# Kernel optimization log

Hardware: AMD Instinct MI355X
Metric: run time of the kernel (lower is better)

## Reference

```python
import jax, jax.numpy as jnp
import numpy as np
import math

B, D, N, H, NHEADS, NCLS = 4096, 256, 256, 1, 4, 10


def conv(x, w, b, stride, pad):
    y = jax.lax.conv_general_dilated(x, w, (stride, stride), [(pad, pad), (pad, pad)],
                                     dimension_numbers=('NCHW', 'OIHW', 'NCHW'))
    return y + b[None, :, None, None]


def cdist(z, c):
    # z: [B, D], c: [N, D] -> Euclidean distance [B, N]
    d2 = jnp.sum(z * z, -1)[:, None] + jnp.sum(c * c, -1)[None, :] - 2.0 * (z @ c.T)
    return jnp.sqrt(jnp.maximum(d2, 0.0))


def setup_inputs() -> dict:
    key = jax.random.key(0)
    ks = jax.random.split(key, 32)
    s = 0.02
    inp = {
        'x': jax.random.normal(ks[0], (B, 3, 32, 32), jnp.float32),
        'y': jax.random.randint(ks[1], (B,), 0, NCLS),
        'conv1_w': jax.random.normal(ks[2], (32, 3, 5, 5), jnp.float32) * s,
        'conv1_b': jnp.zeros((32,), jnp.float32),
        'conv2_w': jax.random.normal(ks[3], (64, 32, 3, 3), jnp.float32) * s,
        'conv2_b': jnp.zeros((64,), jnp.float32),
        'conv3_w': jax.random.normal(ks[4], (128, 64, 3, 3), jnp.float32) * s,
        'conv3_b': jnp.zeros((128,), jnp.float32),
        'conv4_w': jax.random.normal(ks[5], (256, 128, 3, 3), jnp.float32) * s,
        'conv4_b': jnp.zeros((256,), jnp.float32),
        'enc_w': jax.random.normal(ks[6], (256 * 8 * 8, D), jnp.float32) * s,
        'enc_b': jnp.zeros((D,), jnp.float32),
        'class_emb': jax.random.normal(ks[7], (NCLS, D), jnp.float32),
        'node_emb': jax.random.normal(ks[8], (N_NODES := 1, D), jnp.float32),
        'query_w': jax.random.normal(ks[9], (D, D), jnp.float32) * s,
        'query_b': jnp.zeros((D,), jnp.float32),
        'attn_w': jax.random.normal(ks[10], (D, D * NHEADS), jnp.float32) * s,
        'attn_b': jnp.zeros((D * NHEADS,), jnp.float32),
        'clf_w': jax.random.normal(ks[11], (D * NHEADS, NCLS), jnp.float32) * s,
        'clf_b': jnp.zeros((NCLS,), jnp.float32),
        'node_fc_w': jax.random.normal(ks[12], (D, D), jnp.float32) * s,
        'node_fc_b': jnp.zeros((D,), jnp.float32),
        'protos': jax.random.normal(ks[13], (N, D), jnp.float32),
        'grid_pos': jax.random.normal(ks[14], (N, D), jnp.float32),
        'temp_raw': jnp.array([math.log(0.95 / 0.05)], jnp.float32),
        'gate_logits': jnp.zeros((N,), jnp.float32),
    }
    return inp


def reference(x, y, conv1_w, conv1_b, conv2_w, conv2_b, conv3_w, conv3_b,
              conv4_w, conv4_b, enc_w, enc_b, class_emb, node_emb,
              query_w, query_b, attn_w, attn_b, clf_w, clf_b,
              node_fc_w, node_fc_b, protos, grid_pos, temp_raw, gate_logits):
    # shared encoder: conv stack -> flatten -> linear, 32x32 -> 8x8
    h1 = jax.nn.relu(conv(x, conv1_w, conv1_b, 2, 1))    # [B,32,15,15]
    h2 = jax.nn.relu(conv(h1, conv2_w, conv2_b, 2, 1))   # [B,64,8,8]
    h3 = jax.nn.relu(conv(h2, conv3_w, conv3_b, 1, 1))   # [B,128,8,8]
    h4 = jax.nn.relu(conv(h3, conv4_w, conv4_b, 1, 1))   # [B,256,8,8]
    z0 = h4.reshape(x.shape[0], -1) @ enc_w + enc_b      # [B,D]

    # Node: encoder_fc + SoftSOM (cdist + cdist -> softmax -> gate -> renorm -> blend)
    z = z0 @ node_fc_w + node_fc_b
    temp = jax.nn.sigmoid(temp_raw[0]) * (1.0 - 0.001) + 0.001
    d_total = cdist(z, protos) + cdist(z, grid_pos)      # [B,N]
    w = jax.nn.softmax(-d_total / temp, axis=-1) * jax.nn.sigmoid(gate_logits)[None, :]
    w = w / (w.sum(-1, keepdims=True) + 1e-8)
    blended = w @ protos                                 # [B,D]

    # node attention over n_nodes=1
    topo_stack = blended[:, None, :]                     # [B,1,D]
    query = class_emb[y] @ query_w + query_b             # [B,D]
    proj = (node_emb @ attn_w + attn_b).reshape(node_emb.shape[0], NHEADS, D)  # [n,h,D]
    attn_logits = jnp.einsum('bd,nhd->bhn', query, proj)
    attn_w_ = jax.nn.softmax(attn_logits, axis=-1)
    fused = jnp.einsum('bhn,bnd->bhd', attn_w_, topo_stack).reshape(x.shape[0], NHEADS * D)
    logits = fused @ clf_w + clf_b                       # [B,10]
    return logits
```

## Files before the change

kernel.cpp:

```cpp
#include <hip/hip_runtime.h>
#include <math.h>

#define TPB 256

typedef __attribute__((ext_vector_type(8))) short bf16x8;
typedef __attribute__((ext_vector_type(4))) float f32x4;
typedef __attribute__((ext_vector_type(2))) float f32x2;

#define OFF_PN2   0
#define OFF_GN2   256
#define OFF_GATE  512
#define OFF_TEMP  768
#define OFF_WEFF  1024
#define OFF_W1T   3584
#define OFF_W2T_BYTES 737280ul
#define OFF_W3T_BYTES 786432ul
#define OFF_W4T_BYTES 983040ul
#define OFF_EWT_BYTES 2097152ul
#define OFF_NFWT_BYTES 10485760ul
#define OFF_PJD_BYTES  10616832ul
#define OFF_GJD_BYTES  10747904ul
#define OFF_PTB_BYTES  10878976ul
#define OFF_A_BYTES   12582912ul
#define OFF_B_BYTES   (OFF_A_BYTES + 67108864ul)
#define OFF_Z0_BYTES  (OFF_B_BYTES + 33554432ul)

__device__ __forceinline__ float bf2f(ushort u) {
  return __uint_as_float(((unsigned)u) << 16);
}
__device__ __forceinline__ ushort f2bf(float f) {
  unsigned x = __float_as_uint(f);
  return (ushort)((x + 0x7fffu + ((x >> 16) & 1u)) >> 16);
}
__device__ __forceinline__ unsigned pack2(float a, float b) {
  return (unsigned)f2bf(a) | ((unsigned)f2bf(b) << 16);
}

__device__ __forceinline__ void gload_lds16(const ushort* g, ushort* l) {
  __builtin_amdgcn_global_load_lds(
      (const __attribute__((address_space(1))) unsigned int*)g,
      (__attribute__((address_space(3))) unsigned int*)l, 16, 0, 0);
}

__device__ __forceinline__ float block_sum(float v, float* red) {
  #pragma unroll
  for (int off = 32; off > 0; off >>= 1) v += __shfl_down(v, off, 64);
  int wid = threadIdx.x >> 6;
  __syncthreads();
  if ((threadIdx.x & 63) == 0) red[wid] = v;
  __syncthreads();
  return red[0] + red[1] + red[2] + red[3];
}

__global__ void __launch_bounds__(256) k_init(
    const float* __restrict__ ew,    ushort* __restrict__ ewt,
    const float* __restrict__ w1,    const float* __restrict__ w2,
    const float* __restrict__ w3,    const float* __restrict__ w4,
    float* __restrict__ w1t, ushort* __restrict__ w2t,
    ushort* __restrict__ w3t, ushort* __restrict__ w4t,
    const float* __restrict__ protos, const float* __restrict__ gridp,
    const float* __restrict__ gate_logits, const float* __restrict__ temp_raw,
    const float* __restrict__ clf_w, float* __restrict__ ws,
    float* __restrict__ z0,
    const float* __restrict__ nfw, ushort* __restrict__ nfwt,
    ushort* __restrict__ pjd, ushort* __restrict__ gjd,
    ushort* __restrict__ ptb) {
  __shared__ float tile[64][65];
  __shared__ float red[4];
  const int bx = blockIdx.x, t = threadIdx.x;

  if (bx < 1024) {
    int kb = bx & 255, nb = bx >> 8;
    #pragma unroll
    for (int i = 0; i < 16; ++i) {
      int idx = t + i*256, k = idx >> 6, n = idx & 63;
      tile[k][n] = ew[(size_t)(kb*64 + k)*256 + nb*64 + n];
    }
    __syncthreads();
    #pragma unroll
    for (int i = 0; i < 16; ++i) {
      int idx = t + i*256, n = idx >> 6, k = idx & 63;
      ewt[(size_t)(nb*64 + n)*16384 + kb*64 + k] = f2bf(tile[k][n]);
    }
    return;
  }
  if (bx < 2176) {
    int idx = (bx - 1024)*256 + t;
    if (idx < 2400) {
      int tap = idx >> 5, oc = idx & 31;
      w1t[idx] = w1[oc*75 + tap];
    }
    if (idx < 18432) {
      int tap = idx >> 11, r = idx & 2047, oc = r >> 5, ic = r & 31;
      w2t[idx] = f2bf(w2[oc*288 + ic*9 + tap]);
    }
    if (idx < 73728) {
      int tap = idx >> 13, r = idx & 8191, oc = r >> 6, ic = r & 63;
      w3t[idx] = f2bf(w3[oc*576 + ic*9 + tap]);
    }
    if (idx < 294912) {
      int tap = idx >> 15, r = idx & 32767, oc = r >> 7, ic = r & 127;
      w4t[idx] = f2bf(w4[oc*1152 + ic*9 + tap]);
    }
    return;
  }
  if (bx < 2432) {
    int b = bx - 2176;
    #pragma unroll
    for (int u = 0; u < 16; ++u) z0[(size_t)u*65536 + b*256 + t] = 0.f;
    float pv = protos[b*256 + t];
    float gv = gridp [b*256 + t];
    float sp = block_sum(pv*pv, red);
    float sg = block_sum(gv*gv, red);
    if (t == 0) {
      ws[OFF_PN2 + b] = sp;
      ws[OFF_GN2 + b] = sg;
      ws[OFF_GATE + b] = 1.f/(1.f + expf(-gate_logits[b]));
    }
    if (b == 0) {
      for (int i = t; i < 2560; i += TPB) {
        int d = i/10, c = i%10;
        ws[OFF_WEFF + i] = clf_w[d*10+c] + clf_w[(256+d)*10+c]
                         + clf_w[(512+d)*10+c] + clf_w[(768+d)*10+c];
      }
      if (t == 0) {
        float s = 1.f/(1.f + expf(-temp_raw[0]));
        ws[OFF_TEMP] = s*(1.f - 0.001f) + 0.001f;
      }
    }
    return;
  }
  {
    int idx = (bx - 2432)*256 + t;
    int a = idx >> 8, b = idx & 255;
    nfwt[idx] = f2bf(nfw[b*256 + a]);
    pjd [idx] = f2bf(protos[idx]);
    gjd [idx] = f2bf(gridp[idx]);
    ptb [idx] = f2bf(protos[b*256 + a]);
  }
}

__global__ void __launch_bounds__(256) k_conv12(const float* __restrict__ x,
    const float* __restrict__ w1t, const float* __restrict__ b1,
    const ushort* __restrict__ w2t, const float* __restrict__ b2,
    ushort* __restrict__ h2c) {
  __shared__ ushort xs[17*17*40];
  int b = blockIdx.x, t = threadIdx.x;
  for (int i = t; i < 5780; i += TPB) ((unsigned*)xs)[i] = 0u;
  const float* xb = x + (size_t)b*3072;

  if (t < 225) {
    int oy = t/15, ox = t%15;
    f32x2 acc[16];
    #pragma unroll
    for (int o = 0; o < 16; ++o) acc[o] = *(const f32x2*)&b1[2*o];
    for (int ic = 0; ic < 3; ++ic) {
      const int icb = ic*1024;
      #pragma unroll
      for (int ky = 0; ky < 5; ++ky) {
        int iy = 2*oy - 1 + ky;
        bool rok = (unsigned)iy < 32u;
        int rbase = icb + (rok ? iy*32 : 0);
        #pragma unroll
        for (int kx = 0; kx < 5; ++kx) {
          int ix = 2*ox - 1 + kx;
          bool ok = rok && ((unsigned)ix < 32u);
          float xv = xb[rbase + (ok ? ix : 0)];
          xv = ok ? xv : 0.f;
          f32x2 xv2 = {xv, xv};
          const float* wrow = &w1t[(ic*25 + ky*5 + kx)*32];
          #pragma unroll
          for (int g = 0; g < 8; ++g) {
            f32x2 wlo = {wrow[4*g+0], wrow[4*g+1]};
            f32x2 whi = {wrow[4*g+2], wrow[4*g+3]};
            acc[2*g]   += xv2*wlo;
            acc[2*g+1] += xv2*whi;
          }
        }
      }
    }
    unsigned pk[16];
    #pragma unroll
    for (int g = 0; g < 16; ++g)
      pk[g] = pack2(fmaxf(acc[g].x, 0.f), fmaxf(acc[g].y, 0.f));
    ushort* cell = &xs[((oy+1)*17 + (ox+1))*40];
    #pragma unroll
    for (int q = 0; q < 4; ++q) *(uint4*)(cell + q*8) = ((uint4*)pk)[q];
  }
  __syncthreads();

  const int lane = t & 63, w = t >> 6;
  const int quad = lane >> 4, row16 = lane & 15;
  f32x4 acc2[4];
  #pragma unroll
  for (int mt = 0; mt < 4; ++mt) acc2[mt] = (f32x4)0.f;
  #pragma unroll
  for (int ky = 0; ky < 3; ++ky)
    #pragma unroll
    for (int kx = 0; kx < 3; ++kx) {
      int tap = ky*3 + kx;
      bf16x8 bf = *(const bf16x8*)&w2t[tap*2048 + (w*16 + row16)*32 + quad*8];
      #pragma unroll
      for (int mt = 0; mt < 4; ++mt) {
        int px = mt*16 + row16;
        int iy = 2*(px >> 3) + ky, ix = 2*(px & 7) + kx;
        bf16x8 af = *(const bf16x8*)&xs[(iy*17 + ix)*40 + quad*8];
        acc2[mt] = __builtin_amdgcn_mfma_f32_16x16x32_bf16(bf, af, acc2[mt], 0, 0, 0);
      }
    }
  float4 bb = *(const float4*)&b2[w*16 + quad*4];
  #pragma unroll
  for (int mt = 0; mt < 4; ++mt) {
    int px = mt*16 + row16;
    uint2 dd;
    dd.x = pack2(fmaxf(acc2[mt][0] + bb.x, 0.f), fmaxf(acc2[mt][1] + bb.y, 0.f));
    dd.y = pack2(fmaxf(acc2[mt][2] + bb.z, 0.f), fmaxf(acc2[mt][3] + bb.w, 0.f));
    *(uint2*)&h2c[(size_t)b*4096 + px*64 + w*16 + quad*4] = dd;
  }
}

__global__ void __launch_bounds__(256, 2) k_conv34(const ushort* __restrict__ h2c,
    const float* __restrict__ b3, const float* __restrict__ b4,
    const ushort* __restrict__ w3t, const ushort* __restrict__ w4t,
    ushort* __restrict__ h4c, int img_base) {
  __shared__ __attribute__((aligned(16))) ushort buf[27200];
  ushort* xp  = buf;
  ushort* h3p = buf;
  const int bl = blockIdx.x, t = threadIdx.x;

  for (int i = t; i < 648; i += 256) {
    int img = (i >= 324), r = i - img*324;
    int row = r/9, c = r - row*9;
    int rr = (row < 20) ? ((row < 10) ? row : row + 80)
                        : (((row-20) >> 1) + 1)*10 + ((row-20) & 1)*9;
    *(uint4*)&xp[img*7200 + rr*72 + c*8] = (uint4){0,0,0,0};
  }
  #pragma unroll
  for (int u = 0; u < 4; ++u) {
    int i = t + u*256;
    int img = i >> 9, px = (i >> 3) & 63, icg = i & 7;
    bf16x8 v = *(const bf16x8*)&h2c[(size_t)(img_base + bl*2 + img)*4096 + px*64 + icg*8];
    int row = ((px >> 3) + 1)*10 + (px & 7) + 1;
    *(bf16x8*)&xp[img*7200 + row*72 + icg*8] = v;
  }
  __syncthreads();

  const int lane = t & 63, w = t >> 6;
  const int quad = lane >> 4, row16 = lane & 15;

  int b3off[8], b4off[8], r11c[8];
  #pragma unroll
  for (int mt = 0; mt < 8; ++mt) {
    int px = (mt & 3)*16 + row16;
    int r00 = (px >> 3)*10 + (px & 7);
    int img = mt >> 2;
    b3off[mt] = img*7200  + r00*72  + quad*8;
    b4off[mt] = img*13600 + r00*136 + quad*8;
    r11c[mt]  = img*13600 + (r00 + 11)*136;
  }

  const int ocb3 = w*32;
  f32x4 c3[8][2];
  #pragma unroll
  for (int mt = 0; mt < 8; ++mt) { c3[mt][0] = (f32x4)0.f; c3[mt][1] = (f32x4)0.f; }
  const ushort* w3b = w3t + (ocb3 + row16)*64 + quad*8;
  bf16x8 wa0 = *(const bf16x8*)(w3b);
  bf16x8 wa1 = *(const bf16x8*)(w3b + 1024);
  #pragma unroll
  for (int tap = 0; tap < 9; ++tap) {
    const int t72 = ((tap/3)*10 + (tap%3))*72;
    #pragma unroll
    for (int ks = 0; ks < 2; ++ks) {
      const ushort* wn = w3b + ((ks == 0) ? (tap*8192 + 32) : ((tap+1)*8192));
      bf16x8 n0 = *(const bf16x8*)(wn);
      bf16x8 n1 = *(const bf16x8*)(wn + 1024);
      #pragma unroll
      for (int mt = 0; mt < 8; ++mt) {
        bf16x8 af = *(const bf16x8*)&xp[b3off[mt] + t72 + ks*32];
        c3[mt][0] = __builtin_amdgcn_mfma_f32_16x16x32_bf16(wa0, af, c3[mt][0], 0, 0, 0);
        c3[mt][1] = __builtin_amdgcn_mfma_f32_16x16x32_bf16(wa1, af, c3[mt][1], 0, 0, 0);
      }
      wa0 = n0; wa1 = n1;
    }
  }
  __syncthreads();

  for (int i = t; i < 1224; i += 256) {
    int img2 = (i >= 612), r = i - img2*612;
    int row = r/17, c = r - row*17;
    int rr = (row < 20) ? ((row < 10) ? row : row + 80)
                        : (((row-20) >> 1) + 1)*10 + ((row-20) & 1)*9;
    *(uint4*)&h3p[img2*13600 + rr*136 + c*8] = (uint4){0,0,0,0};
  }
  #pragma unroll
  for (int nt = 0; nt < 2; ++nt) {
    float4 bb = *(const float4*)&b3[ocb3 + nt*16 + quad*4];
    #pragma unroll
    for (int mt = 0; mt < 8; ++mt) {
      uint2 dd;
      dd.x = pack2(fmaxf(c3[mt][nt][0] + bb.x, 0.f), fmaxf(c3[mt][nt][1] + bb.y, 0.f));
      dd.y = pack2(fmaxf(c3[mt][nt][2] + bb.z, 0.f), fmaxf(c3[mt][nt][3] + bb.w, 0.f));
      *(uint2*)&h3p[r11c[mt] + ocb3 + nt*16 + quad*4] = dd;
    }
  }
  __syncthreads();

  const int ocb4 = w*64;
  f32x4 c4[8][4];
  #pragma unroll
  for (int mt = 0; mt < 8; ++mt)
    #pragma unroll
    for (int nt = 0; nt < 4; ++nt) c4[mt][nt] = (f32x4)0.f;
  const ushort* w4b = w4t + (ocb4 + row16)*128 + quad*8;
  bf16x8 r4[4];
  #pragma unroll
  for (int nt = 0; nt < 4; ++nt) r4[nt] = *(const bf16x8*)(w4b + nt*2048);
  #pragma unroll
  for (int tap = 0; tap < 9; ++tap) {
    const int t136 = ((tap/3)*10 + (tap%3))*136;
    #pragma unroll
    for (int ks = 0; ks < 4; ++ks) {
      const ushort* wn = w4b + ((ks < 3) ? (tap*32768 + (ks+1)*32) : ((tap+1)*32768));
      bf16x8 nx[4];
      #pragma unroll
      for (int nt = 0; nt < 4; ++nt) nx[nt] = *(const bf16x8*)(wn + nt*2048);
      #pragma unroll
      for (int mt = 0; mt < 8; ++mt) {
        bf16x8 ax = *(const bf16x8*)&h3p[b4off[mt] + t136 + ks*32];
        #pragma unroll
        for (int nt = 0; nt < 4; ++nt)
          c4[mt][nt] = __builtin_amdgcn_mfma_f32_16x16x32_bf16(ax, r4[nt], c4[mt][nt], 0, 0, 0);
      }
      #pragma unroll
      for (int nt = 0; nt < 4; ++nt) r4[nt] = nx[nt];
    }
  }
  #pragma unroll
  for (int nt = 0; nt < 4; ++nt) {
    int oc = ocb4 + nt*16 + row16;
    float bv = b4[oc];
    #pragma unroll
    for (int mt = 0; mt < 8; ++mt) {
      int ig = bl*2 + (mt >> 2);
      int px0 = (mt & 3)*16 + quad*4;
      uint2 dd;
      dd.x = pack2(fmaxf(c4[mt][nt][0] + bv, 0.f), fmaxf(c4[mt][nt][1] + bv, 0.f));
      dd.y = pack2(fmaxf(c4[mt][nt][2] + bv, 0.f), fmaxf(c4[mt][nt][3] + bv, 0.f));
      *(uint2*)&h4c[(size_t)ig*16384 + oc*64 + px0] = dd;
    }
  }
}

__global__ void __launch_bounds__(256) k_enc(const ushort* __restrict__ h4c,
    const ushort* __restrict__ ewt, float* __restrict__ z0, int img_base) {
  __shared__ ushort a_s[128*64];
  __shared__ ushort b_s[128*64];
  const int t = threadIdx.x, bx = blockIdx.x;
  const int slice = bx & 15;
  const int mb = (bx >> 4) & 15;
  const int nb = bx >> 8;
  const int M0 = mb*128, N0 = nb*128;
  const int kbase = slice*1024;
  const int lane = t & 63, wv = t >> 6;
  const int quad = lane >> 4, row16 = lane & 15;
  const int mrow0 = (wv & 1)*64, ncol0 = (wv >> 1)*64;
  const int sr = lane >> 3, sp = lane & 7;

  f32x4 acc[4][4];
  #pragma unroll
  for (int mt = 0; mt < 4; ++mt)
    #pragma unroll
    for (int nt = 0; nt < 4; ++nt) acc[mt][nt] = (f32x4)0.f;

  for (int kt = 0; kt < 16; ++kt) {
    const int k0 = kbase + kt*64;
    __syncthreads();
    #pragma unroll
    for (int u = 0; u < 4; ++u) {
      int r = wv*32 + u*8 + sr;
      int c = sp ^ (r & 7);
      gload_lds16(&h4c[(size_t)(M0 + r)*16384 + k0 + c*8], &a_s[(wv*32 + u*8)*64]);
      gload_lds16(&ewt[(size_t)(N0 + r)*16384 + k0 + c*8], &b_s[(wv*32 + u*8)*64]);
    }
    __syncthreads();
    #pragma unroll
    for (int ks = 0; ks < 2; ++ks) {
      bf16x8 af[4], bf[4];
      #pragma unroll
      for (int mt = 0; mt < 4; ++mt) {
        int r = mrow0 + mt*16 + row16;
        int p = (ks*4 + quad) ^ (r & 7);
        af[mt] = *(const bf16x8*)&a_s[r*64 + p*8];
      }
      #pragma unroll
      for (int nt = 0; nt < 4; ++nt) {
        int r = ncol0 + nt*16 + row16;
        int p = (ks*4 + quad) ^ (r & 7);
        bf[nt] = *(const bf16x8*)&b_s[r*64 + p*8];
      }
      #pragma unroll
      for (int mt = 0; mt < 4; ++mt)
        #pragma unroll
        for (int nt = 0; nt < 4; ++nt)
          acc[mt][nt] = __builtin_amdgcn_mfma_f32_16x16x32_bf16(af[mt], bf[nt], acc[mt][nt], 0, 0, 0);
    }
  }
  #pragma unroll
  for (int mt = 0; mt < 4; ++mt) {
    int mrow = M0 + mrow0 + mt*16 + quad*4;
    #pragma unroll
    for (int nt = 0; nt < 4; ++nt) {
      int col = N0 + ncol0 + nt*16 + row16;
      #pragma unroll
      for (int r = 0; r < 4; ++r)
        atomicAdd(&z0[(size_t)(img_base + mrow + r)*256 + col], acc[mt][nt][r]);
    }
  }
}

__global__ void __launch_bounds__(256) k_post2(const float* __restrict__ z0,
    const float* __restrict__ enc_b, const float* __restrict__ nfb,
    const ushort* __restrict__ nfwt, const ushort* __restrict__ pjd,
    const ushort* __restrict__ gjd, const ushort* __restrict__ ptb,
    const float* __restrict__ ws, const float* __restrict__ clf_b,
    float* __restrict__ out) {
  __shared__ ushort zin[16*264];
  __shared__ ushort zS [16*264];
  __shared__ float  Df [16*264];
  __shared__ ushort wS [16*264];
  __shared__ float  weffS[2560];
  __shared__ float  z2s[16];
  const int t = threadIdx.x, bx = blockIdx.x;
  const int img0 = bx*16;
  #pragma unroll
  for (int u = 0; u < 10; ++u)
    weffS[t + u*256] = ws[OFF_WEFF + t + u*256];
  #pragma unroll
  for (int u = 0; u < 16; ++u) {
    int i = t + u*256;
    int im = i >> 8, d = i & 255;
    zin[im*264 + d] = f2bf(z0[(size_t)(img0 + im)*256 + d] + enc_b[d]);
  }
  __syncthreads();

  const int lane = t & 63, w = t >> 6;
  const int quad = lane >> 4, row16 = lane & 15;
  const int n0 = w*64;

  f32x4 zC[4];
  #pragma unroll
  for (int nt = 0; nt < 4; ++nt) zC[nt] = (f32x4)0.f;
  #pragma unroll
  for (int ks = 0; ks < 8; ++ks) {
    bf16x8 az = *(const bf16x8*)&zin[row16*264 + ks*32 + quad*8];
    #pragma unroll
    for (int nt = 0; nt < 4; ++nt) {
      bf16x8 bw = *(const bf16x8*)&nfwt[(n0 + nt*16 + row16)*256 + ks*32 + quad*8];
      zC[nt] = __builtin_amdgcn_mfma_f32_16x16x32_bf16(az, bw, zC[nt], 0, 0, 0);
    }
  }
  #pragma unroll
  for (int nt = 0; nt < 4; ++nt) {
    int n = n0 + nt*16 + row16;
    float nb = nfb[n];
    #pragma unroll
    for (int r = 0; r < 4; ++r)
      zS[(quad*4 + r)*264 + n] = f2bf(zC[nt][r] + nb);
  }
  __syncthreads();

  {
    int im = t >> 4, jg = t & 15;
    float s = 0.f;
    #pragma unroll
    for (int q = 0; q < 16; ++q) {
      float v = bf2f(zS[im*264 + jg + 16*q]);
      s += v*v;
    }
    #pragma unroll
    for (int off = 8; off; off >>= 1) s += __shfl_xor(s, off, 16);
    if (jg == 0) z2s[im] = s;
  }
  __syncthreads();

  f32x4 dpC[4], dgC[4];
  #pragma unroll
  for (int nt = 0; nt < 4; ++nt) { dpC[nt] = (f32x4)0.f; dgC[nt] = (f32x4)0.f; }
  #pragma unroll
  for (int ks = 0; ks < 8; ++ks) {
    bf16x8 az = *(const bf16x8*)&zS[row16*264 + ks*32 + quad*8];
    #pragma unroll
    for (int nt = 0; nt < 4; ++nt) {
      int j = n0 + nt*16 + row16;
      bf16x8 bp = *(const bf16x8*)&pjd[j*256 + ks*32 + quad*8];
      bf16x8 bg = *(const bf16x8*)&gjd[j*256 + ks*32 + quad*8];
      dpC[nt] = __builtin_amdgcn_mfma_f32_16x16x32_bf16(az, bp, dpC[nt], 0, 0, 0);
      dgC[nt] = __builtin_amdgcn_mfma_f32_16x16x32_bf16(az, bg, dgC[nt], 0, 0, 0);
    }
  }
  {
    float temp = ws[OFF_TEMP];
    #pragma unroll
    for (int nt = 0; nt < 4; ++nt) {
      int j = n0 + nt*16 + row16;
      float pn = ws[OFF_PN2 + j], gn = ws[OFF_GN2 + j];
      #pragma unroll
      for (int r = 0; r < 4; ++r) {
        int im = quad*4 + r;
        float z2 = z2s[im];
        float d2p = z2 + pn - 2.f*dpC[nt][r];
        float d2g = z2 + gn - 2.f*dgC[nt][r];
        float l = -(sqrtf(fmaxf(d2p, 0.f)) + sqrtf(fmaxf(d2g, 0.f)))/temp;
        Df[im*264 + j] = l;
      }
    }
  }
  __syncthreads();

  {
    int im = t >> 4, jg = t & 15;
    float m = -1e30f;
    #pragma unroll
    for (int q = 0; q < 16; ++q) m = fmaxf(m, Df[im*264 + jg + 16*q]);
    #pragma unroll
    for (int off = 8; off; off >>= 1) m = fmaxf(m, __shfl_xor(m, off, 16));
    float E = 0.f, S = 0.f, ev[16], gv[16];
    #pragma unroll
    for (int q = 0; q < 16; ++q) {
      int j = jg + 16*q;
      float e = expf(Df[im*264 + j] - m);
      float g = ws[OFF_GATE + j];
      ev[q] = e; gv[q] = g;
      E += e; S += e*g;
    }
    #pragma unroll
    for (int off = 8; off; off >>= 1) {
      E += __shfl_xor(E, off, 16);
      S += __shfl_xor(S, off, 16);
    }
    float inv = 1.f/(S + 1e-8f*E);
    #pragma unroll
    for (int q = 0; q < 16; ++q)
      wS[im*264 + jg + 16*q] = f2bf(ev[q]*gv[q]*inv);
  }
  __syncthreads();

  f32x4 blC[4];
  #pragma unroll
  for (int nt = 0; nt < 4; ++nt) blC[nt] = (f32x4)0.f;
  #pragma unroll
  for (int ks = 0; ks < 8; ++ks) {
    bf16x8 aw = *(const bf16x8*)&wS[row16*264 + ks*32 + quad*8];
    #pragma unroll
    for (int nt = 0; nt < 4; ++nt) {
      bf16x8 bp = *(const bf16x8*)&ptb[(n0 + nt*16 + row16)*256 + ks*32 + quad*8];
      blC[nt] = __builtin_amdgcn_mfma_f32_16x16x32_bf16(aw, bp, blC[nt], 0, 0, 0);
    }
  }
  #pragma unroll
  for (int nt = 0; nt < 4; ++nt) {
    int d = n0 + nt*16 + row16;
    #pragma unroll
    for (int r = 0; r < 4; ++r)
      Df[(quad*4 + r)*264 + d] = blC[nt][r];
  }
  __syncthreads();

  if (t < 160) {
    int im = t/10, c = t - im*10;
    float s = clf_b[c];
    for (int d = 0; d < 256; ++d)
      s += Df[im*264 + d]*weffS[d*10 + c];
    out[(size_t)(img0 + im)*10 + c] = s;
  }
}

extern "C" void kernel_launch(void* const* d_in, const int* in_sizes, int n_in,
                              void* d_out, int out_size, void* d_ws, size_t ws_size,
                              hipStream_t stream) {
  (void)in_sizes; (void)n_in; (void)out_size; (void)ws_size;
  const float* x      = (const float*)d_in[0];
  const float* c1w    = (const float*)d_in[2];
  const float* c1b    = (const float*)d_in[3];
  const float* c2w    = (const float*)d_in[4];
  const float* c2b    = (const float*)d_in[5];
  const float* c3w    = (const float*)d_in[6];
  const float* c3b    = (const float*)d_in[7];
  const float* c4w    = (const float*)d_in[8];
  const float* c4b    = (const float*)d_in[9];
  const float* encw   = (const float*)d_in[10];
  const float* encb   = (const float*)d_in[11];
  const float* clfw   = (const float*)d_in[18];
  const float* clfb   = (const float*)d_in[19];
  const float* nfw    = (const float*)d_in[20];
  const float* nfb    = (const float*)d_in[21];
  const float* protos = (const float*)d_in[22];
  const float* gridp  = (const float*)d_in[23];
  const float* traw   = (const float*)d_in[24];
  const float* gatel  = (const float*)d_in[25];

  float*  ws   = (float*)d_ws;
  float*  w1t  = ws + OFF_W1T;
  ushort* w2t  = (ushort*)((char*)d_ws + OFF_W2T_BYTES);
  ushort* w3t  = (ushort*)((char*)d_ws + OFF_W3T_BYTES);
  ushort* w4t  = (ushort*)((char*)d_ws + OFF_W4T_BYTES);
  ushort* ewt  = (ushort*)((char*)d_ws + OFF_EWT_BYTES);
  ushort* nfwt = (ushort*)((char*)d_ws + OFF_NFWT_BYTES);
  ushort* pjd  = (ushort*)((char*)d_ws + OFF_PJD_BYTES);
  ushort* gjd  = (ushort*)((char*)d_ws + OFF_GJD_BYTES);
  ushort* ptb  = (ushort*)((char*)d_ws + OFF_PTB_BYTES);
  ushort* h4c  = (ushort*)((char*)d_ws + OFF_A_BYTES);
  ushort* h2c  = (ushort*)((char*)d_ws + OFF_B_BYTES);
  float*  z0   = (float*) ((char*)d_ws + OFF_Z0_BYTES);
  float*  out  = (float*)d_out;

  hipLaunchKernelGGL(k_init, dim3(2688), dim3(TPB), 0, stream,
                     encw, ewt, c1w, c2w, c3w, c4w, w1t, w2t, w3t, w4t,
                     protos, gridp, gatel, traw, clfw, ws, z0,
                     nfw, nfwt, pjd, gjd, ptb);
  hipLaunchKernelGGL(k_conv12, dim3(4096), dim3(TPB), 0, stream, x, w1t, c1b, w2t, c2b, h2c);
  for (int c = 0; c < 2; ++c) {
    hipLaunchKernelGGL(k_conv34, dim3(1024), dim3(TPB), 0, stream,
                       h2c, c3b, c4b, w3t, w4t, h4c, c*2048);
    hipLaunchKernelGGL(k_enc, dim3(512), dim3(TPB), 0, stream, h4c, ewt, z0, c*2048);
  }
  hipLaunchKernelGGL(k_post2, dim3(256), dim3(TPB), 0, stream,
                     z0, encb, nfb, nfwt, pjd, gjd, ptb, ws, clfb, out);
}
```

Baseline: 524.6 us.

## Double-buffer encoder GEMM LDS tiles, swizzle block order, cache post constants in LDS

The encoder split-K GEMM now double-buffers its LDS tiles, so the next K tile's global-to-LDS loads are issued while MFMAs run on the current tile. This also drops one barrier per iteration. The block index mapping is reordered so that consecutive blocks share the same M tile across slices and N blocks, which should improve L2 reuse. In k_post2, the gate, prototype-norm and grid-norm vectors are staged in shared memory instead of being re-read from global memory. The cost is twice the LDS per encoder block, which may lower occupancy.

```diff
diff --git a/kernel.cpp b/kernel.cpp
--- a/kernel.cpp
+++ b/kernel.cpp
@@ -353,12 +353,13 @@
 
 __global__ void __launch_bounds__(256) k_enc(const ushort* __restrict__ h4c,
     const ushort* __restrict__ ewt, float* __restrict__ z0, int img_base) {
-  __shared__ ushort a_s[128*64];
-  __shared__ ushort b_s[128*64];
-  const int t = threadIdx.x, bx = blockIdx.x;
-  const int slice = bx & 15;
-  const int mb = (bx >> 4) & 15;
-  const int nb = bx >> 8;
+  __shared__ ushort a_s[2][128*64];
+  __shared__ ushort b_s[2][128*64];
+  const int t = threadIdx.x, bid = blockIdx.x;
+  const int grp = (bid & 7) + ((bid >> 7) << 3);
+  const int slice = grp & 15;
+  const int nb    = grp >> 4;
+  const int mb    = (bid >> 3) & 15;
   const int M0 = mb*128, N0 = nb*128;
   const int kbase = slice*1024;
   const int lane = t & 63, wv = t >> 6;
@@ -372,17 +373,27 @@
     #pragma unroll
     for (int nt = 0; nt < 4; ++nt) acc[mt][nt] = (f32x4)0.f;
 
+  #pragma unroll
+  for (int u = 0; u < 4; ++u) {
+    int r = wv*32 + u*8 + sr;
+    int c = sp ^ (r & 7);
+    gload_lds16(&h4c[(size_t)(M0 + r)*16384 + kbase + c*8], &a_s[0][(wv*32 + u*8)*64]);
+    gload_lds16(&ewt[(size_t)(N0 + r)*16384 + kbase + c*8], &b_s[0][(wv*32 + u*8)*64]);
+  }
+  __syncthreads();
+
+  int cur = 0;
   for (int kt = 0; kt < 16; ++kt) {
-    const int k0 = kbase + kt*64;
-    __syncthreads();
-    #pragma unroll
-    for (int u = 0; u < 4; ++u) {
-      int r = wv*32 + u*8 + sr;
-      int c = sp ^ (r & 7);
-      gload_lds16(&h4c[(size_t)(M0 + r)*16384 + k0 + c*8], &a_s[(wv*32 + u*8)*64]);
-      gload_lds16(&ewt[(size_t)(N0 + r)*16384 + k0 + c*8], &b_s[(wv*32 + u*8)*64]);
-    }
-    __syncthreads();
+    if (kt < 15) {
+      const int k1 = kbase + (kt + 1)*64;
+      #pragma unroll
+      for (int u = 0; u < 4; ++u) {
+        int r = wv*32 + u*8 + sr;
+        int c = sp ^ (r & 7);
+        gload_lds16(&h4c[(size_t)(M0 + r)*16384 + k1 + c*8], &a_s[cur^1][(wv*32 + u*8)*64]);
+        gload_lds16(&ewt[(size_t)(N0 + r)*16384 + k1 + c*8], &b_s[cur^1][(wv*32 + u*8)*64]);
+      }
+    }
     #pragma unroll
     for (int ks = 0; ks < 2; ++ks) {
       bf16x8 af[4], bf[4];
@@ -390,13 +401,13 @@
       for (int mt = 0; mt < 4; ++mt) {
         int r = mrow0 + mt*16 + row16;
         int p = (ks*4 + quad) ^ (r & 7);
-        af[mt] = *(const bf16x8*)&a_s[r*64 + p*8];
+        af[mt] = *(const bf16x8*)&a_s[cur][r*64 + p*8];
       }
       #pragma unroll
       for (int nt = 0; nt < 4; ++nt) {
         int r = ncol0 + nt*16 + row16;
         int p = (ks*4 + quad) ^ (r & 7);
-        bf[nt] = *(const bf16x8*)&b_s[r*64 + p*8];
+        bf[nt] = *(const bf16x8*)&b_s[cur][r*64 + p*8];
       }
       #pragma unroll
       for (int mt = 0; mt < 4; ++mt)
@@ -404,6 +415,8 @@
         for (int nt = 0; nt < 4; ++nt)
           acc[mt][nt] = __builtin_amdgcn_mfma_f32_16x16x32_bf16(af[mt], bf[nt], acc[mt][nt], 0, 0, 0);
     }
+    __syncthreads();
+    cur ^= 1;
   }
   #pragma unroll
   for (int mt = 0; mt < 4; ++mt) {
@@ -429,9 +442,13 @@
   __shared__ float  Df [16*264];
   __shared__ ushort wS [16*264];
   __shared__ float  weffS[2560];
+  __shared__ float  gateS[256], pnS[256], gnS[256];
   __shared__ float  z2s[16];
   const int t = threadIdx.x, bx = blockIdx.x;
   const int img0 = bx*16;
+  gateS[t] = ws[OFF_GATE + t];
+  pnS[t]   = ws[OFF_PN2 + t];
+  gnS[t]   = ws[OFF_GN2 + t];
   #pragma unroll
   for (int u = 0; u < 10; ++u)
     weffS[t + u*256] = ws[OFF_WEFF + t + u*256];
@@ -503,7 +520,7 @@
     #pragma unroll
     for (int nt = 0; nt < 4; ++nt) {
       int j = n0 + nt*16 + row16;
-      float pn = ws[OFF_PN2 + j], gn = ws[OFF_GN2 + j];
+      float pn = pnS[j], gn = gnS[j];
       #pragma unroll
       for (int r = 0; r < 4; ++r) {
         int im = quad*4 + r;
@@ -529,7 +546,7 @@
     for (int q = 0; q < 16; ++q) {
       int j = jg + 16*q;
       float e = expf(Df[im*264 + j] - m);
-      float g = ws[OFF_GATE + j];
+      float g = gateS[j];
       ev[q] = e; gv[q] = g;
       E += e; S += e*g;
     }
```

After: 520.1 us. About the same (-0.8%).
